# Performance work log

Hardware: AMD Instinct MI355X
Metric: run time of the kernel (lower is better)

The kernel has to match this reference:

```python
import jax, jax.numpy as jnp
import numpy as np

INPUT_DIM = 256
EMBED_DIM = 256
NUM_HEADS = 8
HEAD_DIM = EMBED_DIM // NUM_HEADS
N_TOKENS = 11136
N_BATCH = 16


def _xavier(key, shape):
    fan_out, fan_in = shape
    bound = np.sqrt(6.0 / (fan_in + fan_out)).astype(np.float32)
    return jax.random.uniform(key, shape, jnp.float32, -bound, bound)


def setup_inputs() -> dict:
    key = jax.random.key(0)
    k_x, k_ids, k_qkv, k_o = jax.random.split(key, 4)
    x = jax.random.normal(k_x, (N_TOKENS, INPUT_DIM), jnp.float32)
    batch_ids = jnp.sort(jax.random.randint(k_ids, (N_TOKENS,), 0, N_BATCH)).astype(jnp.int32)
    qkv_w = _xavier(k_qkv, (3 * EMBED_DIM, INPUT_DIM))
    qkv_b = jnp.zeros((3 * EMBED_DIM,), jnp.float32)
    o_w = _xavier(k_o, (EMBED_DIM, EMBED_DIM))
    o_b = jnp.zeros((EMBED_DIM,), jnp.float32)
    return {"x": x, "batch_ids": batch_ids, "qkv_w": qkv_w, "qkv_b": qkv_b,
            "o_w": o_w, "o_b": o_b}


def reference(x, batch_ids, qkv_w, qkv_b, o_w, o_b):
    # batch_ids is concrete metadata (mirrors np.unique on CPU in the original).
    ids = np.asarray(batch_ids)
    vals, counts = np.unique(ids, return_counts=True)
    B = len(vals)
    S = int(counts.max())
    offsets = np.concatenate([np.zeros(1, np.int64), np.cumsum(counts)[:-1]])
    seg = np.searchsorted(vals, ids)               # segment index per token
    pos = np.arange(ids.shape[0]) - offsets[seg]   # position within segment

    qkv = x @ qkv_w.T + qkv_b                      # [N, 3E]
    # pad_sequence with padding_value=1 -> scatter tokens into an all-ones buffer
    fin = jnp.ones((B, S, 3 * EMBED_DIM), qkv.dtype).at[seg, pos].set(qkv)
    # padded rows sum to exactly 3E (all ones) -> mask True marks padding
    pad_mask = fin.sum(-1) >= fin.shape[-1]        # [B, S]

    qkv4 = fin.reshape(B, S, NUM_HEADS, 3 * HEAD_DIM).transpose(0, 2, 1, 3)
    q, k, v = jnp.split(qkv4, 3, axis=-1)          # each [B, H, S, hd]

    logits = jnp.einsum('bhqd,bhkd->bhqk', q, k) * (HEAD_DIM ** -0.5)
    logits = jnp.where(pad_mask[:, None, None, :], -jnp.inf, logits)
    attn = jax.nn.softmax(logits, axis=-1)         # [B, H, S, S]

    out = jnp.einsum('bhqk,bhkd->bhqd', attn, v)
    out = out.transpose(0, 2, 1, 3).reshape(B, S, EMBED_DIM)
    out = out[seg, pos]                            # unpad -> [N, E]
    return out @ o_w.T + o_b
```

## Files before the change

kernel.cpp:

```cpp
#include <hip/hip_runtime.h>
#include <stdint.h>


#define N_TOK 11136
#define E 256
#define H 8
#define HD 32

typedef __attribute__((ext_vector_type(8))) __bf16 bf16x8;
typedef __attribute__((ext_vector_type(8))) unsigned short u16x8;
typedef __attribute__((ext_vector_type(4))) float f32x4;

__device__ __forceinline__ unsigned short f2bf(float f) {
  unsigned int u = __float_as_uint(f);
  u = (u + 0x7FFFu + ((u >> 16) & 1u)) >> 16;
  return (unsigned short)u;
}
__device__ __forceinline__ float bf2f(unsigned short s) {
  return __uint_as_float(((unsigned int)s) << 16);
}
__device__ __forceinline__ bf16x8 ld8(const unsigned short* p) {
  return *(const bf16x8*)p;
}

__global__ void k_offsets(const int* __restrict__ ids, int* __restrict__ offs) {
  int b = threadIdx.x;
  if (b > 16) return;
  int lo = 0, hi = N_TOK;
  while (lo < hi) { int mid = (lo + hi) >> 1; if (ids[mid] < b) lo = mid + 1; else hi = mid; }
  offs[b] = lo;
}

__global__ void k_split(const float* __restrict__ x, const float* __restrict__ qw,
                        const float* __restrict__ ow,
                        unsigned short* __restrict__ xhi, unsigned short* __restrict__ xlo,
                        unsigned short* __restrict__ whi, unsigned short* __restrict__ wlo,
                        unsigned short* __restrict__ owb) {
  const int NX4 = N_TOK * E / 4;
  const int NW4 = 3 * E * E / 4;
  const int NO4 = E * E / 4;
  int total = NX4 + NW4 + NO4;
  for (int i = blockIdx.x * blockDim.x + threadIdx.x; i < total;
       i += gridDim.x * blockDim.x) {
    if (i < NX4) {
      float4 v = ((const float4*)x)[i];
      ushort4 hv, lv;
      hv.x = f2bf(v.x); lv.x = f2bf(v.x - bf2f(hv.x));
      hv.y = f2bf(v.y); lv.y = f2bf(v.y - bf2f(hv.y));
      hv.z = f2bf(v.z); lv.z = f2bf(v.z - bf2f(hv.z));
      hv.w = f2bf(v.w); lv.w = f2bf(v.w - bf2f(hv.w));
      ((ushort4*)xhi)[i] = hv; ((ushort4*)xlo)[i] = lv;
    } else if (i < NX4 + NW4) {
      int j = i - NX4;
      float4 v = ((const float4*)qw)[j];
      ushort4 hv, lv;
      hv.x = f2bf(v.x); lv.x = f2bf(v.x - bf2f(hv.x));
      hv.y = f2bf(v.y); lv.y = f2bf(v.y - bf2f(hv.y));
      hv.z = f2bf(v.z); lv.z = f2bf(v.z - bf2f(hv.z));
      hv.w = f2bf(v.w); lv.w = f2bf(v.w - bf2f(hv.w));
      ((ushort4*)whi)[j] = hv; ((ushort4*)wlo)[j] = lv;
    } else {
      int j = i - NX4 - NW4;
      float4 v = ((const float4*)ow)[j];
      ushort4 hv;
      hv.x = f2bf(v.x); hv.y = f2bf(v.y); hv.z = f2bf(v.z); hv.w = f2bf(v.w);
      ((ushort4*)owb)[j] = hv;
    }
  }
}

#define QK_BSTRIDE 264
#define QSCALE (0.17677669529663687f * 1.4426950408889634f)
__global__ __launch_bounds__(256, 3) void k_qkv(
    const unsigned short* __restrict__ xhi, const unsigned short* __restrict__ xlo,
    const unsigned short* __restrict__ whi, const unsigned short* __restrict__ wlo,
    const float* __restrict__ qkv_b,
    unsigned short* __restrict__ Qb, unsigned short* __restrict__ Kb,
    unsigned short* __restrict__ Vt) {
  __shared__ __align__(16) unsigned short Bhi[48 * QK_BSTRIDE];
  __shared__ __align__(16) unsigned short Blo[48 * QK_BSTRIDE];
  int tid = threadIdx.x;
  int w = tid >> 6, lane = tid & 63, m = lane & 15, quad = lane >> 4;
  int col0 = blockIdx.x * 48;
  int base0 = blockIdx.y * 128;

  {
    const u16x8* wh8 = (const u16x8*)(whi + (size_t)col0 * E);
    const u16x8* wl8 = (const u16x8*)(wlo + (size_t)col0 * E);
#pragma unroll
    for (int i = 0; i < 6; ++i) {
      int flat = i * 256 + tid;
      int row = flat >> 5, c8 = flat & 31;
      *(u16x8*)(Bhi + row * QK_BSTRIDE + c8 * 8) = wh8[flat];
      *(u16x8*)(Blo + row * QK_BSTRIDE + c8 * 8) = wl8[flat];
    }
  }
  __syncthreads();

  f32x4 acc[2][3] = {};
  for (int kc = 0; kc < 8; ++kc) {
    int ko = kc * 32 + quad * 8;
    bf16x8 ah[2], al[2];
#pragma unroll
    for (int mt = 0; mt < 2; ++mt) {
      int arow = base0 + mt * 64 + w * 16 + m;
      ah[mt] = ld8(xhi + (size_t)arow * E + ko);
      al[mt] = ld8(xlo + (size_t)arow * E + ko);
    }
#pragma unroll
    for (int t = 0; t < 3; ++t) {
      bf16x8 bh = ld8(Bhi + (16 * t + m) * QK_BSTRIDE + ko);
      bf16x8 bl = ld8(Blo + (16 * t + m) * QK_BSTRIDE + ko);
#pragma unroll
      for (int mt = 0; mt < 2; ++mt) {
        acc[mt][t] = __builtin_amdgcn_mfma_f32_16x16x32_bf16(ah[mt], bh, acc[mt][t], 0, 0, 0);
        acc[mt][t] = __builtin_amdgcn_mfma_f32_16x16x32_bf16(ah[mt], bl, acc[mt][t], 0, 0, 0);
        acc[mt][t] = __builtin_amdgcn_mfma_f32_16x16x32_bf16(al[mt], bh, acc[mt][t], 0, 0, 0);
      }
    }
  }
#pragma unroll
  for (int t = 0; t < 3; ++t) {
    int j = col0 + 16 * t + m;
    int hd = j / 96;
    int rr = j - hd * 96;
    float bias = qkv_b[j];
#pragma unroll
    for (int mt = 0; mt < 2; ++mt) {
      int tokb = base0 + mt * 64 + w * 16 + quad * 4;
      if (rr < 64) {
        float qsc = (rr < 32) ? QSCALE : 1.0f;
        unsigned short* dst = (rr < 32) ? (Qb + (size_t)hd * N_TOK * HD + rr)
                                        : (Kb + (size_t)hd * N_TOK * HD + (rr - 32));
#pragma unroll
        for (int r = 0; r < 4; ++r)
          dst[(size_t)(tokb + r) * HD] = f2bf((acc[mt][t][r] + bias) * qsc);
      } else {
        int d = rr - 64;
        ushort4 pk;
        pk.x = f2bf(acc[mt][t][0] + bias); pk.y = f2bf(acc[mt][t][1] + bias);
        pk.z = f2bf(acc[mt][t][2] + bias); pk.w = f2bf(acc[mt][t][3] + bias);
        *(ushort4*)(Vt + (size_t)(hd * HD + d) * N_TOK + tokb) = pk;
      }
    }
  }
}

#define PSTRIDE 72
__global__ __launch_bounds__(256, 4) void k_attn(
    const int* __restrict__ ids, const int* __restrict__ offs,
    const unsigned short* __restrict__ Qb, const unsigned short* __restrict__ Kb,
    const unsigned short* __restrict__ Vt,
    unsigned short* __restrict__ attnb) {
  __shared__ __align__(16) unsigned short Kl[2][64 * 32];
  __shared__ __align__(16) unsigned short Vl[2][32 * 64];
  __shared__ __align__(16) unsigned short ldsP[4][16 * PSTRIDE];
  __shared__ int bred[8];
  int tid = threadIdx.x;
  int w = tid >> 6, lane = tid & 63;
  int m = lane & 15, quad = lane >> 4;
  int h = blockIdx.y;
  int tok0 = blockIdx.x * 64;
  int q0 = tok0 + w * 16;
  unsigned short* P = ldsP[w];
  int tok = q0 + m;
  int b = ids[tok];
  int st = offs[b], en = offs[b + 1];
  int kmin = st, kmax = en, stM = st, enm = en;
#pragma unroll
  for (int d = 1; d <= 8; d <<= 1) {
    kmin = min(kmin, __shfl_xor(kmin, d));
    kmax = max(kmax, __shfl_xor(kmax, d));
    stM  = max(stM,  __shfl_xor(stM,  d));
    enm  = min(enm,  __shfl_xor(enm,  d));
  }
  if (lane == 0) { bred[w] = kmin; bred[4 + w] = kmax; }
  __syncthreads();
  int kminB = min(min(bred[0], bred[1]), min(bred[2], bred[3]));
  int kmaxB = max(max(bred[4], bred[5]), max(bred[6], bred[7]));
  int k0beg = kminB & ~63;

  const unsigned short* Kbase = Kb + (size_t)h * N_TOK * HD;
  const unsigned short* Vbase = Vt + (size_t)h * HD * N_TOK;
  bf16x8 qf = ld8(Qb + (size_t)(h * N_TOK + tok) * HD + quad * 8);

  int krow = w * 16 + (lane >> 2);
  int kgof = (lane & 3) * 8;
  int vrow = w * 8 + (lane >> 3);
  int vgof = (lane & 7) * 8;

  bf16x8 kg = ld8(Kbase + (size_t)(k0beg + krow) * HD + kgof);
  bf16x8 vg = ld8(Vbase + (size_t)vrow * N_TOK + k0beg + vgof);
  *(bf16x8*)(&Kl[0][krow * 32 + kgof]) = kg;
  *(bf16x8*)(&Vl[0][vrow * 64 + vgof]) = vg;
  __syncthreads();

  float lsum = 0.f;
  f32x4 o0 = {}, o1 = {};
  int buf = 0;
  for (int k0 = k0beg; k0 < kmaxB; k0 += 64) {
    int k1 = (k0 + 64 < kmaxB) ? (k0 + 64) : k0;
    kg = ld8(Kbase + (size_t)(k1 + krow) * HD + kgof);
    vg = ld8(Vbase + (size_t)vrow * N_TOK + k1 + vgof);
    const unsigned short* Kc = &Kl[buf][0];
    const unsigned short* Vc = &Vl[buf][0];
    f32x4 s[4];
#pragma unroll
    for (int i = 0; i < 4; ++i) {
      bf16x8 kf = ld8(Kc + (16 * i + m) * 32 + quad * 8);
      f32x4 z = {};
      s[i] = __builtin_amdgcn_mfma_f32_16x16x32_bf16(kf, qf, z, 0, 0, 0);
    }
    bool interior = (k0 >= stM && k0 + 64 <= enm);
    int jb = k0 + quad * 4;
#pragma unroll
    for (int i = 0; i < 4; ++i) {
      float p[4];
#pragma unroll
      for (int r = 0; r < 4; ++r) {
        float sv = s[i][r];
        if (!interior) {
          int j = jb + 16 * i + r;
          sv = (j >= st && j < en) ? sv : -3e38f;
        }
        float e;
        asm("v_exp_f32 %0, %1" : "=v"(e) : "v"(sv));
        p[r] = e;
      }
      lsum += (p[0] + p[1]) + (p[2] + p[3]);
      unsigned int b0 = __float_as_uint(p[0]) + 0x8000u;
      unsigned int b1 = __float_as_uint(p[1]) + 0x8000u;
      unsigned int b2 = __float_as_uint(p[2]) + 0x8000u;
      unsigned int b3 = __float_as_uint(p[3]) + 0x8000u;
      uint2 pk;
      pk.x = (b1 & 0xFFFF0000u) | (b0 >> 16);
      pk.y = (b3 & 0xFFFF0000u) | (b2 >> 16);
      *(uint2*)(P + m * PSTRIDE + 16 * i + quad * 4) = pk;
    }
#pragma unroll
    for (int c = 0; c < 2; ++c) {
      bf16x8 pf  = ld8(P + m * PSTRIDE + 32 * c + quad * 8);
      bf16x8 vf0 = ld8(Vc + m * 64 + 32 * c + quad * 8);
      bf16x8 vf1 = ld8(Vc + (16 + m) * 64 + 32 * c + quad * 8);
      o0 = __builtin_amdgcn_mfma_f32_16x16x32_bf16(vf0, pf, o0, 0, 0, 0);
      o1 = __builtin_amdgcn_mfma_f32_16x16x32_bf16(vf1, pf, o1, 0, 0, 0);
    }
    *(bf16x8*)(&Kl[buf ^ 1][krow * 32 + kgof]) = kg;
    *(bf16x8*)(&Vl[buf ^ 1][vrow * 64 + vgof]) = vg;
    __syncthreads();
    buf ^= 1;
  }
  lsum += __shfl_xor(lsum, 16);
  lsum += __shfl_xor(lsum, 32);
  float inv = 1.0f / lsum;
  ushort4 pk0, pk1;
  pk0.x = f2bf(o0[0] * inv); pk0.y = f2bf(o0[1] * inv);
  pk0.z = f2bf(o0[2] * inv); pk0.w = f2bf(o0[3] * inv);
  pk1.x = f2bf(o1[0] * inv); pk1.y = f2bf(o1[1] * inv);
  pk1.z = f2bf(o1[2] * inv); pk1.w = f2bf(o1[3] * inv);
  *(ushort4*)(attnb + (size_t)tok * E + h * HD + quad * 4) = pk0;
  *(ushort4*)(attnb + (size_t)tok * E + h * HD + 16 + quad * 4) = pk1;
}

__global__ __launch_bounds__(256, 2) void k_oproj(
    const unsigned short* __restrict__ attnb, const unsigned short* __restrict__ owb,
    const float* __restrict__ ob, float* __restrict__ out) {
  __shared__ __align__(16) unsigned short Bo[64 * QK_BSTRIDE];
  int tid = threadIdx.x;
  int w = tid >> 6, lane = tid & 63, m = lane & 15, quad = lane >> 4;
  int tok0 = blockIdx.x * 64, col0 = blockIdx.y * 64;
  {
    const u16x8* o8 = (const u16x8*)(owb + (size_t)col0 * E);
#pragma unroll
    for (int i = 0; i < 8; ++i) {
      int flat = i * 256 + tid;
      int row = flat >> 5, c8 = flat & 31;
      *(u16x8*)(Bo + row * QK_BSTRIDE + c8 * 8) = o8[flat];
    }
  }
  __syncthreads();
  f32x4 acc[4] = {};
  int arow = tok0 + 16 * w + m;
  for (int kc = 0; kc < 8; ++kc) {
    int ko = kc * 32 + quad * 8;
    bf16x8 a = ld8(attnb + (size_t)arow * E + ko);
#pragma unroll
    for (int t = 0; t < 4; ++t) {
      bf16x8 b = ld8(Bo + (16 * t + m) * QK_BSTRIDE + ko);
      acc[t] = __builtin_amdgcn_mfma_f32_16x16x32_bf16(a, b, acc[t], 0, 0, 0);
    }
  }
#pragma unroll
  for (int t = 0; t < 4; ++t) {
    int j = col0 + 16 * t + m;
    float bias = ob[j];
#pragma unroll
    for (int r = 0; r < 4; ++r) {
      int tok = tok0 + 16 * w + quad * 4 + r;
      out[(size_t)tok * E + j] = acc[t][r] + bias;
    }
  }
}

extern "C" void kernel_launch(void* const* d_in, const int* in_sizes, int n_in,
                              void* d_out, int out_size, void* d_ws, size_t ws_size,
                              hipStream_t stream) {
  const float* x   = (const float*)d_in[0];
  const int*   ids = (const int*)d_in[1];
  const float* qw  = (const float*)d_in[2];
  const float* qb  = (const float*)d_in[3];
  const float* ow  = (const float*)d_in[4];
  const float* ob  = (const float*)d_in[5];
  float* out = (float*)d_out;

  char* p = (char*)d_ws;
  auto alloc = [&](size_t bytes) {
    char* r = p;
    p += (bytes + 255) & ~(size_t)255;
    return r;
  };
  int* offs = (int*)alloc(32 * sizeof(int));
  unsigned short* xhi = (unsigned short*)alloc((size_t)N_TOK * E * 2);
  unsigned short* xlo = (unsigned short*)alloc((size_t)N_TOK * E * 2);
  unsigned short* whi = (unsigned short*)alloc((size_t)3 * E * E * 2);
  unsigned short* wlo = (unsigned short*)alloc((size_t)3 * E * E * 2);
  unsigned short* owb = (unsigned short*)alloc((size_t)E * E * 2);
  unsigned short* Qb  = (unsigned short*)alloc((size_t)N_TOK * E * 2);
  unsigned short* Kb  = (unsigned short*)alloc((size_t)N_TOK * E * 2);
  unsigned short* Vt  = (unsigned short*)alloc((size_t)N_TOK * E * 2);
  unsigned short* att = (unsigned short*)alloc((size_t)N_TOK * E * 2);

  k_offsets<<<dim3(1), dim3(64), 0, stream>>>(ids, offs);
  k_split<<<dim3(1712), dim3(256), 0, stream>>>(x, qw, ow, xhi, xlo, whi, wlo, owb);
  k_qkv<<<dim3(16, N_TOK / 128), dim3(256), 0, stream>>>(xhi, xlo, whi, wlo, qb, Qb, Kb, Vt);
  k_attn<<<dim3(N_TOK / 64, H), dim3(256), 0, stream>>>(ids, offs, Qb, Kb, Vt, att);
  k_oproj<<<dim3(N_TOK / 64, E / 64), dim3(256), 0, stream>>>(att, owb, ob, out);
}
```

Measured before the change: 157.2 us.

## Fuse offsets into split kernel, enlarge QKV row tile, prefetch A operands

Folds the segment-offset binary search into the first block of the split kernel, removing one kernel launch. The QKV GEMM now gives each wave 48 rows (192 per block) and register double-buffers the x hi/lo fragments so the next k-chunk's global loads overlap the current MFMAs. The output projection also prefetches its A fragment one chunk ahead, and its launch bounds rise to 4 blocks per SM. The cost is more registers per thread in the QKV kernel and fewer blocks in its grid.

```diff
diff --git a/kernel.cpp b/kernel.cpp
--- a/kernel.cpp
+++ b/kernel.cpp
@@ -23,19 +23,16 @@
   return *(const bf16x8*)p;
 }
 
-__global__ void k_offsets(const int* __restrict__ ids, int* __restrict__ offs) {
-  int b = threadIdx.x;
-  if (b > 16) return;
-  int lo = 0, hi = N_TOK;
-  while (lo < hi) { int mid = (lo + hi) >> 1; if (ids[mid] < b) lo = mid + 1; else hi = mid; }
-  offs[b] = lo;
-}
-
 __global__ void k_split(const float* __restrict__ x, const float* __restrict__ qw,
-                        const float* __restrict__ ow,
+                        const float* __restrict__ ow, const int* __restrict__ ids,
                         unsigned short* __restrict__ xhi, unsigned short* __restrict__ xlo,
                         unsigned short* __restrict__ whi, unsigned short* __restrict__ wlo,
-                        unsigned short* __restrict__ owb) {
+                        unsigned short* __restrict__ owb, int* __restrict__ offs) {
+  if (blockIdx.x == 0 && threadIdx.x < 17) {
+    int b = threadIdx.x, lo = 0, hi = N_TOK;
+    while (lo < hi) { int mid = (lo + hi) >> 1; if (ids[mid] < b) lo = mid + 1; else hi = mid; }
+    offs[b] = lo;
+  }
   const int NX4 = N_TOK * E / 4;
   const int NW4 = 3 * E * E / 4;
   const int NO4 = E * E / 4;
@@ -82,7 +79,7 @@
   int tid = threadIdx.x;
   int w = tid >> 6, lane = tid & 63, m = lane & 15, quad = lane >> 4;
   int col0 = blockIdx.x * 48;
-  int base0 = blockIdx.y * 128;
+  int rowb = blockIdx.y * 192 + w * 48;
 
   {
     const u16x8* wh8 = (const u16x8*)(whi + (size_t)col0 * E);
@@ -97,22 +94,32 @@
   }
   __syncthreads();
 
-  f32x4 acc[2][3] = {};
+  f32x4 acc[3][3] = {};
+  bf16x8 ahn[3], aln[3];
+#pragma unroll
+  for (int mt = 0; mt < 3; ++mt) {
+    const size_t ro = (size_t)(rowb + mt * 16 + m) * E + quad * 8;
+    ahn[mt] = ld8(xhi + ro);
+    aln[mt] = ld8(xlo + ro);
+  }
   for (int kc = 0; kc < 8; ++kc) {
+    bf16x8 ah[3], al[3];
+#pragma unroll
+    for (int mt = 0; mt < 3; ++mt) { ah[mt] = ahn[mt]; al[mt] = aln[mt]; }
+    int kon = (kc < 7 ? kc + 1 : kc) * 32 + quad * 8;
+#pragma unroll
+    for (int mt = 0; mt < 3; ++mt) {
+      const size_t ro = (size_t)(rowb + mt * 16 + m) * E + kon;
+      ahn[mt] = ld8(xhi + ro);
+      aln[mt] = ld8(xlo + ro);
+    }
     int ko = kc * 32 + quad * 8;
-    bf16x8 ah[2], al[2];
-#pragma unroll
-    for (int mt = 0; mt < 2; ++mt) {
-      int arow = base0 + mt * 64 + w * 16 + m;
-      ah[mt] = ld8(xhi + (size_t)arow * E + ko);
-      al[mt] = ld8(xlo + (size_t)arow * E + ko);
-    }
 #pragma unroll
     for (int t = 0; t < 3; ++t) {
       bf16x8 bh = ld8(Bhi + (16 * t + m) * QK_BSTRIDE + ko);
       bf16x8 bl = ld8(Blo + (16 * t + m) * QK_BSTRIDE + ko);
 #pragma unroll
-      for (int mt = 0; mt < 2; ++mt) {
+      for (int mt = 0; mt < 3; ++mt) {
         acc[mt][t] = __builtin_amdgcn_mfma_f32_16x16x32_bf16(ah[mt], bh, acc[mt][t], 0, 0, 0);
         acc[mt][t] = __builtin_amdgcn_mfma_f32_16x16x32_bf16(ah[mt], bl, acc[mt][t], 0, 0, 0);
         acc[mt][t] = __builtin_amdgcn_mfma_f32_16x16x32_bf16(al[mt], bh, acc[mt][t], 0, 0, 0);
@@ -126,8 +133,8 @@
     int rr = j - hd * 96;
     float bias = qkv_b[j];
 #pragma unroll
-    for (int mt = 0; mt < 2; ++mt) {
-      int tokb = base0 + mt * 64 + w * 16 + quad * 4;
+    for (int mt = 0; mt < 3; ++mt) {
+      int tokb = rowb + mt * 16 + quad * 4;
       if (rr < 64) {
         float qsc = (rr < 32) ? QSCALE : 1.0f;
         unsigned short* dst = (rr < 32) ? (Qb + (size_t)hd * N_TOK * HD + rr)
@@ -262,7 +269,7 @@
   *(ushort4*)(attnb + (size_t)tok * E + h * HD + 16 + quad * 4) = pk1;
 }
 
-__global__ __launch_bounds__(256, 2) void k_oproj(
+__global__ __launch_bounds__(256, 4) void k_oproj(
     const unsigned short* __restrict__ attnb, const unsigned short* __restrict__ owb,
     const float* __restrict__ ob, float* __restrict__ out) {
   __shared__ __align__(16) unsigned short Bo[64 * QK_BSTRIDE];
@@ -281,9 +288,12 @@
   __syncthreads();
   f32x4 acc[4] = {};
   int arow = tok0 + 16 * w + m;
+  const unsigned short* abase = attnb + (size_t)arow * E + quad * 8;
+  bf16x8 an = ld8(abase);
   for (int kc = 0; kc < 8; ++kc) {
+    bf16x8 a = an;
+    an = ld8(abase + (kc < 7 ? kc + 1 : kc) * 32);
     int ko = kc * 32 + quad * 8;
-    bf16x8 a = ld8(attnb + (size_t)arow * E + ko);
 #pragma unroll
     for (int t = 0; t < 4; ++t) {
       bf16x8 b = ld8(Bo + (16 * t + m) * QK_BSTRIDE + ko);
@@ -330,9 +340,8 @@
   unsigned short* Vt  = (unsigned short*)alloc((size_t)N_TOK * E * 2);
   unsigned short* att = (unsigned short*)alloc((size_t)N_TOK * E * 2);
 
-  k_offsets<<<dim3(1), dim3(64), 0, stream>>>(ids, offs);
-  k_split<<<dim3(1712), dim3(256), 0, stream>>>(x, qw, ow, xhi, xlo, whi, wlo, owb);
-  k_qkv<<<dim3(16, N_TOK / 128), dim3(256), 0, stream>>>(xhi, xlo, whi, wlo, qb, Qb, Kb, Vt);
+  k_split<<<dim3(1712), dim3(256), 0, stream>>>(x, qw, ow, ids, xhi, xlo, whi, wlo, owb, offs);
+  k_qkv<<<dim3(16, N_TOK / 192), dim3(256), 0, stream>>>(xhi, xlo, whi, wlo, qb, Qb, Kb, Vt);
   k_attn<<<dim3(N_TOK / 64, H), dim3(256), 0, stream>>>(ids, offs, Qb, Kb, Vt, att);
   k_oproj<<<dim3(N_TOK / 64, E / 64), dim3(256), 0, stream>>>(att, owb, ob, out);
 }
```

After: 159.8 us. About the same (+1.7%).
